# Performance work log

Measured on AMD Instinct MI355X. Metric: run time of the kernel, lower is better.

The kernel has to match this reference:

```python
import jax, jax.numpy as jnp
import numpy as np

E = 8      # num_experts
K = 2      # top-k
HID = 2048 # per-expert hidden dim


def setup_inputs() -> dict:
    key = jax.random.key(0)
    ks = jax.random.split(key, 7)
    D = 1024
    x = jax.random.normal(ks[0], (4, 2048, D), dtype=jnp.float32)
    Wr = jax.random.normal(ks[1], (D, E), dtype=jnp.float32) * 0.02
    br = jnp.zeros((E,), jnp.float32)
    W1 = jax.random.normal(ks[2], (E, D, 2 * HID), dtype=jnp.float32) * 0.02
    b1 = jnp.zeros((E, 2 * HID), jnp.float32)
    W2 = jax.random.normal(ks[3], (E, HID, D), dtype=jnp.float32) * 0.02
    b2 = jnp.zeros((E, D), jnp.float32)
    return {"x": x, "Wr": Wr, "br": br, "W1": W1, "b1": b1, "W2": W2, "b2": b2}


def reference(x, Wr, br, W1, b1, W2, b2):
    B, T, D = x.shape
    xf = x.reshape(-1, D)                               # [N, D]

    # --- router ---
    logits = xf @ Wr + br                               # [N, E]
    probs = jax.nn.softmax(logits, axis=-1)
    topk_val, topk_idx = jax.lax.top_k(logits, K)       # [N, K]
    scores = jax.nn.softmax(topk_val, axis=-1)          # [N, K]

    # --- load-balancing aux loss ---
    one_hot = jax.nn.one_hot(topk_idx, E, dtype=jnp.float32)   # [N, K, E]
    f = one_hot.sum(axis=1).mean(axis=0)                # [E] fraction routed
    p = probs.mean(axis=0)                              # [E] mean prob
    aux_loss = E * jnp.sum(jax.lax.stop_gradient(f) * p)

    # --- every expert over all tokens (faithful to naive module) ---
    h = jnp.einsum('nd,edh->enh', xf, W1) + b1[:, None, :]     # [E, N, 2H]
    a, b = h[..., :HID], h[..., HID:]
    g = jax.nn.silu(a) * b                              # swiglu, [E, N, H]
    oe = jnp.einsum('enh,ehd->end', g, W2) + b2[:, None, :]    # [E, N, D]

    # --- combine: gather each token's top-k expert outputs, weight, sum ---
    oe = oe.transpose(1, 0, 2)                          # [N, E, D]
    sel = jnp.take_along_axis(oe, topk_idx[:, :, None], axis=1)  # [N, K, D]
    out = (sel * scores[:, :, None]).sum(axis=1)        # [N, D]

    return out.reshape(B, T, D), aux_loss
```

## Files before the change

### kernel.cpp

```cpp
#include <hip/hip_runtime.h>
#include <hip/hip_bf16.h>
#include <math.h>

typedef __attribute__((ext_vector_type(8))) __bf16 bh8;
typedef __attribute__((ext_vector_type(4))) float  f4;

#define NTOK   8192
#define DIM    1024
#define HIDK   2048

#define OFF_CNT    0
#define OFF_PSUM   64
#define OFF_OFFS   128
#define OFF_ROWS   512
#define OFF_GATES  (512+262144)
#define OFF_XBF    524800
#define OFF_G      (524800+16777216)
#define OFF_W1S    (OFF_G + 68157440)
#define OFF_W2S    (OFF_W1S + 67108864)

__device__ __forceinline__ unsigned short f2bf(float x){
    union { float f; unsigned u; } v; v.f = x;
    unsigned r = v.u + 0x7FFFu + ((v.u >> 16) & 1u);
    return (unsigned short)(r >> 16);
}
__device__ __forceinline__ unsigned pk2(float a, float b){
    return (unsigned)f2bf(a) | ((unsigned)f2bf(b) << 16);
}
__device__ __forceinline__ void gload_lds16(const void* g, void* l){
    __builtin_amdgcn_global_load_lds((const __attribute__((address_space(1))) void*)g,
                                     (__attribute__((address_space(3))) void*)l, 16, 0, 0);
}

__global__ void convert_x(const float* __restrict__ x, short* __restrict__ xbf){
    size_t i = ((size_t)blockIdx.x * 256 + threadIdx.x) * 8;
    const float4* s = (const float4*)(x + i);
    float4 a = s[0], b = s[1];
    uint4 u;
    u.x = pk2(a.x, a.y); u.y = pk2(a.z, a.w);
    u.z = pk2(b.x, b.y); u.w = pk2(b.z, b.w);
    *(uint4*)(xbf + i) = u;
}

__global__ void prep_w(const float* __restrict__ W, short* __restrict__ Ws,
                       int Kdim, int Ndim){
    int kb = blockIdx.x, nb = blockIdx.y, e = blockIdx.z;
    int KB = Kdim >> 5, NB = Ndim >> 7;
    __shared__ float tile[32 * 132];
    int t = threadIdx.x;
    const float* src = W + ((size_t)(e * Kdim + kb * 32)) * Ndim + (size_t)nb * 128;
    #pragma unroll
    for (int l = 0; l < 4; l++){
        int flat = (l * 256 + t) * 4;
        int k = flat >> 7, n = flat & 127;
        float4 v = *(const float4*)(src + (size_t)k * Ndim + n);
        float* d = &tile[k * 132 + n];
        d[0] = v.x; d[1] = v.y; d[2] = v.z; d[3] = v.w;
    }
    __syncthreads();
    short* dst = Ws + (((size_t)(e * NB + nb)) * KB + kb) * 4096;
    uint out[8];
    #pragma unroll
    for (int sl = 0; sl < 2; sl++){
        int s = t * 2 + sl;
        int nl = s >> 2, pos = s & 3;
        int c = pos ^ (nl & 3) ^ ((nl >> 2) & 3);
        #pragma unroll
        for (int jj = 0; jj < 4; jj++){
            float a = tile[(c * 8 + jj * 2) * 132 + nl];
            float b = tile[(c * 8 + jj * 2 + 1) * 132 + nl];
            out[sl * 4 + jj] = pk2(a, b);
        }
    }
    *(uint4*)(dst + t * 16)     = *(uint4*)&out[0];
    *(uint4*)(dst + t * 16 + 8) = *(uint4*)&out[4];
}

__global__ void router(const float* __restrict__ x, const float* __restrict__ Wr,
                       const float* __restrict__ br,
                       int* cnt, float* psum, int* rows, float* gates){
    __shared__ float pP[8];
    __shared__ int   tE[32][2];
    __shared__ float tS[32][2];
    __shared__ int   lcnt[8], lpos[64], lexp[64], gbase[8];
    int t = threadIdx.x, lane = t & 63, w = t >> 6;
    if (t < 8){ pP[t] = 0.f; lcnt[t] = 0; }
    __syncthreads();
    int n0 = blockIdx.x * 32 + w * 8;
    for (int tk = 0; tk < 8; tk++){
        int n = n0 + tk;
        float acc[8] = {0,0,0,0,0,0,0,0};
        const float* xr = x + (size_t)n * DIM;
        for (int d = lane; d < DIM; d += 64){
            float xv = xr[d];
            const float* wrow = Wr + d * 8;
            #pragma unroll
            for (int e = 0; e < 8; e++) acc[e] += xv * wrow[e];
        }
        #pragma unroll
        for (int e = 0; e < 8; e++){
            float v = acc[e];
            v += __shfl_xor(v, 32); v += __shfl_xor(v, 16); v += __shfl_xor(v, 8);
            v += __shfl_xor(v, 4);  v += __shfl_xor(v, 2);  v += __shfl_xor(v, 1);
            acc[e] = v;
        }
        if (lane == 0){
            float l[8], ex[8], m = -1e30f;
            #pragma unroll
            for (int e = 0; e < 8; e++){ l[e] = acc[e] + br[e]; m = fmaxf(m, l[e]); }
            float s = 0.f;
            #pragma unroll
            for (int e = 0; e < 8; e++){ ex[e] = expf(l[e] - m); s += ex[e]; }
            float inv = 1.f / s;
            #pragma unroll
            for (int e = 0; e < 8; e++) atomicAdd(&pP[e], ex[e] * inv);
            int i0 = 0; float v0 = l[0];
            #pragma unroll
            for (int e = 1; e < 8; e++) if (l[e] > v0){ v0 = l[e]; i0 = e; }
            int i1 = -1; float v1 = -1e30f;
            #pragma unroll
            for (int e = 0; e < 8; e++) if (e != i0 && l[e] > v1){ v1 = l[e]; i1 = e; }
            float s0 = 1.f / (1.f + expf(v1 - v0));
            int ti = w * 8 + tk;
            tE[ti][0] = i0; tE[ti][1] = i1;
            tS[ti][0] = s0; tS[ti][1] = 1.f - s0;
        }
    }
    __syncthreads();
    if (t < 64){
        int e = tE[t >> 1][t & 1];
        lexp[t] = e;
        lpos[t] = atomicAdd(&lcnt[e], 1);
    }
    __syncthreads();
    if (t < 8){
        gbase[t] = atomicAdd(&cnt[t], lcnt[t]);
        atomicAdd(&psum[t], pP[t]);
    }
    __syncthreads();
    if (t < 64){
        int e = lexp[t];
        int p = gbase[e] + lpos[t];
        int n = blockIdx.x * 32 + (t >> 1);
        rows[e * NTOK + p]  = n;
        gates[e * NTOK + p] = tS[t >> 1][t & 1];
    }
}

__global__ void finalize_aux(const int* cnt, const float* psum, int* offs, float* out_aux){
    if (threadIdx.x == 0){
        int off = 0; float aux = 0.f;
        for (int e = 0; e < 8; e++){
            offs[e] = off; off += cnt[e];
            aux += ((float)cnt[e] * (1.f/8192.f)) * (psum[e] * (1.f/8192.f));
        }
        out_aux[0] = 8.f * aux;
    }
}

__global__ __launch_bounds__(256, 4) void gemm1(
    const short* __restrict__ xbf, const short* __restrict__ W1s,
    const float* __restrict__ b1, const int* __restrict__ cnt,
    const int* __restrict__ offs, const int* __restrict__ rows,
    short* __restrict__ g)
{
    int e = blockIdx.z;
    int Me = cnt[e];
    int mbase = blockIdx.y << 7;
    if (mbase >= Me) return;
    int xB = blockIdx.x;
    __shared__ short As[128 * 32];
    __shared__ short Bsa[64 * 32];
    __shared__ short Bsb[64 * 32];

    int t = threadIdx.x, lane = t & 63, w = t >> 6;
    int wr = w & 1, wc = w >> 1;
    int m = lane & 15, q = lane >> 4;
    int sw8 = (q ^ (m & 3) ^ ((m >> 2) & 3)) << 3;

    const int* rowsE = rows + (e << 13) + mbase;
    int r = t >> 2, pos = t & 3;
    int ca = pos ^ (r & 3) ^ ((r >> 2) & 3);
    int tok0 = (mbase + r      < Me) ? rowsE[r]      : 0;
    int tok1 = (mbase + r + 64 < Me) ? rowsE[r + 64] : 0;
    const short* ga0 = xbf + ((size_t)tok0 << 10) + (ca << 3);
    const short* ga1 = xbf + ((size_t)tok1 << 10) + (ca << 3);
    int ha = xB & 1, nb128 = xB >> 1;
    const short* gb0 = W1s + ((size_t)((e * 32 + nb128)      * 32)) * 4096 + (ha * 256 + t) * 8;
    const short* gb1 = W1s + ((size_t)((e * 32 + 16 + nb128) * 32)) * 4096 + (ha * 256 + t) * 8;
    short* ldsA0 = As  + w * 512;
    short* ldsA1 = As  + 2048 + w * 512;
    short* ldsBa = Bsa + w * 512;
    short* ldsBb = Bsb + w * 512;

    f4 acc_a[4][2], acc_b[4][2];
    f4 zz = {0.f,0.f,0.f,0.f};
    #pragma unroll
    for (int i = 0; i < 4; i++)
        #pragma unroll
        for (int j = 0; j < 2; j++){ acc_a[i][j] = zz; acc_b[i][j] = zz; }

    for (int k0 = 0; k0 < DIM; k0 += 32){
        __syncthreads();
        gload_lds16(ga0, ldsA0);
        gload_lds16(ga1, ldsA1);
        gload_lds16(gb0, ldsBa);
        gload_lds16(gb1, ldsBb);
        ga0 += 32; ga1 += 32; gb0 += 4096; gb1 += 4096;
        __syncthreads();
        bh8 av[4], ba[2], bb[2];
        #pragma unroll
        for (int i = 0; i < 4; i++)
            av[i] = *(const bh8*)&As[(wr*64 + i*16 + m) * 32 + sw8];
        #pragma unroll
        for (int j = 0; j < 2; j++){
            int nn = ((wc << 5) + j*16 + m) * 32 + sw8;
            ba[j] = *(const bh8*)&Bsa[nn];
            bb[j] = *(const bh8*)&Bsb[nn];
        }
        #pragma unroll
        for (int i = 0; i < 4; i++)
            #pragma unroll
            for (int j = 0; j < 2; j++){
                acc_a[i][j] = __builtin_amdgcn_mfma_f32_16x16x32_bf16(av[i], ba[j], acc_a[i][j], 0, 0, 0);
                acc_b[i][j] = __builtin_amdgcn_mfma_f32_16x16x32_bf16(av[i], bb[j], acc_b[i][j], 0, 0, 0);
            }
    }
    int c0 = xB << 6;
    const float* b1e = b1 + (e << 12);
    int colb = (wc << 5) + m;
    float vba[2], vbb[2];
    #pragma unroll
    for (int j = 0; j < 2; j++){
        vba[j] = b1e[c0 + colb + j*16];
        vbb[j] = b1e[HIDK + c0 + colb + j*16];
    }
    int rb = wr * 64 + (q << 2);
    short* gE = g + ((size_t)(offs[e] + mbase)) * HIDK;
    #pragma unroll
    for (int i = 0; i < 4; i++)
        #pragma unroll
        for (int reg = 0; reg < 4; reg++){
            int mr = rb + i*16 + reg;
            if (mbase + mr < Me){
                short* grow = gE + (size_t)mr * HIDK + c0 + colb;
                #pragma unroll
                for (int j = 0; j < 2; j++){
                    float va = acc_a[i][j][reg] + vba[j];
                    float vb = acc_b[i][j][reg] + vbb[j];
                    grow[j*16] = (short)f2bf(va / (1.f + __expf(-va)) * vb);
                }
            }
        }
}

__global__ __launch_bounds__(256, 4) void gemm2(
    const short* __restrict__ g, const short* __restrict__ W2s,
    const float* __restrict__ b2, const int* __restrict__ cnt,
    const int* __restrict__ offs, const int* __restrict__ rows,
    const float* __restrict__ gates, float* __restrict__ out)
{
    int e = blockIdx.z;
    int Me = cnt[e];
    int mbase = blockIdx.y << 7;
    if (mbase >= Me) return;
    int db = blockIdx.x;
    __shared__ short As[128 * 32];
    __shared__ short Bs[128 * 32];

    int t = threadIdx.x, lane = t & 63, w = t >> 6;
    int wr = w & 1, wc = w >> 1;
    int m = lane & 15, q = lane >> 4;
    int sw8 = (q ^ (m & 3) ^ ((m >> 2) & 3)) << 3;

    int gbaseR = offs[e] + mbase;
    int r = t >> 2;
    int ca = (t & 3) ^ (r & 3) ^ ((r >> 2) & 3);
    const short* ga0 = g + ((size_t)(gbaseR + r))      * HIDK + (ca << 3);
    const short* ga1 = g + ((size_t)(gbaseR + r + 64)) * HIDK + (ca << 3);
    const short* gb0 = W2s + ((size_t)((e * 8 + db) * 64)) * 4096 + t * 8;
    const short* gb1 = gb0 + 2048;
    short* ldsA0 = As + w * 512;
    short* ldsA1 = As + 2048 + w * 512;
    short* ldsB0 = Bs + w * 512;
    short* ldsB1 = Bs + 2048 + w * 512;

    f4 acc[4][4];
    f4 zz = {0.f,0.f,0.f,0.f};
    #pragma unroll
    for (int i = 0; i < 4; i++)
        #pragma unroll
        for (int j = 0; j < 4; j++) acc[i][j] = zz;

    for (int k0 = 0; k0 < HIDK; k0 += 32){
        __syncthreads();
        gload_lds16(ga0, ldsA0);
        gload_lds16(ga1, ldsA1);
        gload_lds16(gb0, ldsB0);
        gload_lds16(gb1, ldsB1);
        ga0 += 32; ga1 += 32; gb0 += 4096; gb1 += 4096;
        __syncthreads();
        bh8 av[4], bv[4];
        #pragma unroll
        for (int i = 0; i < 4; i++)
            av[i] = *(const bh8*)&As[(wr*64 + i*16 + m) * 32 + sw8];
        #pragma unroll
        for (int j = 0; j < 4; j++)
            bv[j] = *(const bh8*)&Bs[(wc*64 + j*16 + m) * 32 + sw8];
        #pragma unroll
        for (int i = 0; i < 4; i++)
            #pragma unroll
            for (int j = 0; j < 4; j++)
                acc[i][j] = __builtin_amdgcn_mfma_f32_16x16x32_bf16(av[i], bv[j], acc[i][j], 0, 0, 0);
    }
    int d0 = db << 7;
    const float* b2e = b2 + (e << 10);
    int colb = wc * 64 + m;
    float vb2[4];
    #pragma unroll
    for (int j = 0; j < 4; j++) vb2[j] = b2e[d0 + colb + j*16];
    const int* rowsE = rows + (e << 13) + mbase;
    const float* gatesE = gates + (e << 13) + mbase;
    int rb = wr * 64 + (q << 2);
    #pragma unroll
    for (int i = 0; i < 4; i++)
        #pragma unroll
        for (int reg = 0; reg < 4; reg++){
            int mr = rb + i*16 + reg;
            if (mbase + mr < Me){
                int token = rowsE[mr];
                float gate = gatesE[mr];
                float* orow = out + ((size_t)token << 10) + d0 + colb;
                #pragma unroll
                for (int j = 0; j < 4; j++)
                    unsafeAtomicAdd(&orow[j*16], gate * (acc[i][j][reg] + vb2[j]));
            }
        }
}

extern "C" void kernel_launch(void* const* d_in, const int* in_sizes, int n_in,
                              void* d_out, int out_size, void* d_ws, size_t ws_size,
                              hipStream_t stream) {
    const float* x  = (const float*)d_in[0];
    const float* Wr = (const float*)d_in[1];
    const float* br = (const float*)d_in[2];
    const float* W1 = (const float*)d_in[3];
    const float* b1 = (const float*)d_in[4];
    const float* W2 = (const float*)d_in[5];
    const float* b2 = (const float*)d_in[6];
    float* out = (float*)d_out;

    char* ws = (char*)d_ws;
    int*   cnt   = (int*)(ws + OFF_CNT);
    float* psum  = (float*)(ws + OFF_PSUM);
    int*   offs  = (int*)(ws + OFF_OFFS);
    int*   rows  = (int*)(ws + OFF_ROWS);
    float* gates = (float*)(ws + OFF_GATES);
    short* xbf   = (short*)(ws + OFF_XBF);
    short* g     = (short*)(ws + OFF_G);
    short* W1s   = (short*)(ws + OFF_W1S);
    short* W2s   = (short*)(ws + OFF_W2S);

    hipMemsetAsync(ws, 0, 192, stream);
    hipMemsetAsync(d_out, 0, (size_t)NTOK * DIM * 4, stream);

    prep_w<<<dim3(32, 32, 8), 256, 0, stream>>>(W1, W1s, 1024, 4096);
    prep_w<<<dim3(64, 8, 8),  256, 0, stream>>>(W2, W2s, 2048, 1024);
    convert_x<<<4096, 256, 0, stream>>>(x, xbf);
    router<<<256, 256, 0, stream>>>(x, Wr, br, cnt, psum, rows, gates);
    finalize_aux<<<1, 64, 0, stream>>>(cnt, psum, offs, out + (size_t)NTOK * DIM);
    gemm1<<<dim3(32, 64, 8), 256, 0, stream>>>(xbf, W1s, b1, cnt, offs, rows, g);
    gemm2<<<dim3(8, 64, 8),  256, 0, stream>>>(g, W2s, b2, cnt, offs, rows, gates, out);
}
```

Measured before the change: 673.9 us.

## Double-buffer LDS tiles in both expert GEMMs to overlap loads with MFMA

Both grouped GEMM kernels now keep two LDS buffers per operand and prefetch the next K-slice with global_load_lds while the MFMAs run on the current slice. The two __syncthreads per iteration become an inline-asm s_waitcnt vmcnt(4) plus s_barrier, and a bare barrier after compute. This is meant to hide global-memory latency behind compute. It doubles LDS use, which can lower occupancy under launch_bounds(256,4), and it depends on the hand-written vmcnt count matching the four outstanding loads per thread.

```diff
diff --git a/kernel.cpp b/kernel.cpp
--- a/kernel.cpp
+++ b/kernel.cpp
@@ -31,6 +31,9 @@
     __builtin_amdgcn_global_load_lds((const __attribute__((address_space(1))) void*)g,
                                      (__attribute__((address_space(3))) void*)l, 16, 0, 0);
 }
+#define WAITBAR_PREV() asm volatile("s_waitcnt vmcnt(4)\n\ts_barrier" ::: "memory")
+#define WAITBAR_ALL()  asm volatile("s_waitcnt vmcnt(0)\n\ts_barrier" ::: "memory")
+#define BAR_ONLY()     asm volatile("s_barrier" ::: "memory")
 
 __global__ void convert_x(const float* __restrict__ x, short* __restrict__ xbf){
     size_t i = ((size_t)blockIdx.x * 256 + threadIdx.x) * 8;
@@ -169,9 +172,9 @@
     int mbase = blockIdx.y << 7;
     if (mbase >= Me) return;
     int xB = blockIdx.x;
-    __shared__ short As[128 * 32];
-    __shared__ short Bsa[64 * 32];
-    __shared__ short Bsb[64 * 32];
+    __shared__ short As [2][4096];
+    __shared__ short Bsa[2][2048];
+    __shared__ short Bsb[2][2048];
 
     int t = threadIdx.x, lane = t & 63, w = t >> 6;
     int wr = w & 1, wc = w >> 1;
@@ -188,10 +191,10 @@
     int ha = xB & 1, nb128 = xB >> 1;
     const short* gb0 = W1s + ((size_t)((e * 32 + nb128)      * 32)) * 4096 + (ha * 256 + t) * 8;
     const short* gb1 = W1s + ((size_t)((e * 32 + 16 + nb128) * 32)) * 4096 + (ha * 256 + t) * 8;
-    short* ldsA0 = As  + w * 512;
-    short* ldsA1 = As  + 2048 + w * 512;
-    short* ldsBa = Bsa + w * 512;
-    short* ldsBb = Bsb + w * 512;
+    short* ldsA0 = &As [0][w * 512];
+    short* ldsA1 = &As [0][2048 + w * 512];
+    short* ldsBa = &Bsa[0][w * 512];
+    short* ldsBb = &Bsb[0][w * 512];
 
     f4 acc_a[4][2], acc_b[4][2];
     f4 zz = {0.f,0.f,0.f,0.f};
@@ -200,23 +203,53 @@
         #pragma unroll
         for (int j = 0; j < 2; j++){ acc_a[i][j] = zz; acc_b[i][j] = zz; }
 
-    for (int k0 = 0; k0 < DIM; k0 += 32){
-        __syncthreads();
-        gload_lds16(ga0, ldsA0);
-        gload_lds16(ga1, ldsA1);
-        gload_lds16(gb0, ldsBa);
-        gload_lds16(gb1, ldsBb);
+    gload_lds16(ga0, ldsA0);
+    gload_lds16(ga1, ldsA1);
+    gload_lds16(gb0, ldsBa);
+    gload_lds16(gb1, ldsBb);
+    ga0 += 32; ga1 += 32; gb0 += 4096; gb1 += 4096;
+
+    int cur = 0;
+    #pragma unroll 2
+    for (int k0 = 0; k0 < DIM - 32; k0 += 32){
+        int nxt = cur ^ 1;
+        gload_lds16(ga0, ldsA0 + nxt * 4096);
+        gload_lds16(ga1, ldsA1 + nxt * 4096);
+        gload_lds16(gb0, ldsBa + nxt * 2048);
+        gload_lds16(gb1, ldsBb + nxt * 2048);
         ga0 += 32; ga1 += 32; gb0 += 4096; gb1 += 4096;
-        __syncthreads();
+        WAITBAR_PREV();
         bh8 av[4], ba[2], bb[2];
         #pragma unroll
         for (int i = 0; i < 4; i++)
-            av[i] = *(const bh8*)&As[(wr*64 + i*16 + m) * 32 + sw8];
+            av[i] = *(const bh8*)&As[cur][(wr*64 + i*16 + m) * 32 + sw8];
         #pragma unroll
         for (int j = 0; j < 2; j++){
             int nn = ((wc << 5) + j*16 + m) * 32 + sw8;
-            ba[j] = *(const bh8*)&Bsa[nn];
-            bb[j] = *(const bh8*)&Bsb[nn];
+            ba[j] = *(const bh8*)&Bsa[cur][nn];
+            bb[j] = *(const bh8*)&Bsb[cur][nn];
+        }
+        #pragma unroll
+        for (int i = 0; i < 4; i++)
+            #pragma unroll
+            for (int j = 0; j < 2; j++){
+                acc_a[i][j] = __builtin_amdgcn_mfma_f32_16x16x32_bf16(av[i], ba[j], acc_a[i][j], 0, 0, 0);
+                acc_b[i][j] = __builtin_amdgcn_mfma_f32_16x16x32_bf16(av[i], bb[j], acc_b[i][j], 0, 0, 0);
+            }
+        BAR_ONLY();
+        cur = nxt;
+    }
+    WAITBAR_ALL();
+    {
+        bh8 av[4], ba[2], bb[2];
+        #pragma unroll
+        for (int i = 0; i < 4; i++)
+            av[i] = *(const bh8*)&As[cur][(wr*64 + i*16 + m) * 32 + sw8];
+        #pragma unroll
+        for (int j = 0; j < 2; j++){
+            int nn = ((wc << 5) + j*16 + m) * 32 + sw8;
+            ba[j] = *(const bh8*)&Bsa[cur][nn];
+            bb[j] = *(const bh8*)&Bsb[cur][nn];
         }
         #pragma unroll
         for (int i = 0; i < 4; i++)
@@ -265,8 +298,8 @@
     int mbase = blockIdx.y << 7;
     if (mbase >= Me) return;
     int db = blockIdx.x;
-    __shared__ short As[128 * 32];
-    __shared__ short Bs[128 * 32];
+    __shared__ short As[2][4096];
+    __shared__ short Bs[2][4096];
 
     int t = threadIdx.x, lane = t & 63, w = t >> 6;
     int wr = w & 1, wc = w >> 1;
@@ -280,10 +313,10 @@
     const short* ga1 = g + ((size_t)(gbaseR + r + 64)) * HIDK + (ca << 3);
     const short* gb0 = W2s + ((size_t)((e * 8 + db) * 64)) * 4096 + t * 8;
     const short* gb1 = gb0 + 2048;
-    short* ldsA0 = As + w * 512;
-    short* ldsA1 = As + 2048 + w * 512;
-    short* ldsB0 = Bs + w * 512;
-    short* ldsB1 = Bs + 2048 + w * 512;
+    short* ldsA0 = &As[0][w * 512];
+    short* ldsA1 = &As[0][2048 + w * 512];
+    short* ldsB0 = &Bs[0][w * 512];
+    short* ldsB1 = &Bs[0][2048 + w * 512];
 
     f4 acc[4][4];
     f4 zz = {0.f,0.f,0.f,0.f};
@@ -292,21 +325,46 @@
         #pragma unroll
         for (int j = 0; j < 4; j++) acc[i][j] = zz;
 
-    for (int k0 = 0; k0 < HIDK; k0 += 32){
-        __syncthreads();
-        gload_lds16(ga0, ldsA0);
-        gload_lds16(ga1, ldsA1);
-        gload_lds16(gb0, ldsB0);
-        gload_lds16(gb1, ldsB1);
+    gload_lds16(ga0, ldsA0);
+    gload_lds16(ga1, ldsA1);
+    gload_lds16(gb0, ldsB0);
+    gload_lds16(gb1, ldsB1);
+    ga0 += 32; ga1 += 32; gb0 += 4096; gb1 += 4096;
+
+    int cur = 0;
+    #pragma unroll 2
+    for (int k0 = 0; k0 < HIDK - 32; k0 += 32){
+        int nxt = cur ^ 1;
+        gload_lds16(ga0, ldsA0 + nxt * 4096);
+        gload_lds16(ga1, ldsA1 + nxt * 4096);
+        gload_lds16(gb0, ldsB0 + nxt * 4096);
+        gload_lds16(gb1, ldsB1 + nxt * 4096);
         ga0 += 32; ga1 += 32; gb0 += 4096; gb1 += 4096;
-        __syncthreads();
+        WAITBAR_PREV();
         bh8 av[4], bv[4];
         #pragma unroll
         for (int i = 0; i < 4; i++)
-            av[i] = *(const bh8*)&As[(wr*64 + i*16 + m) * 32 + sw8];
+            av[i] = *(const bh8*)&As[cur][(wr*64 + i*16 + m) * 32 + sw8];
         #pragma unroll
         for (int j = 0; j < 4; j++)
-            bv[j] = *(const bh8*)&Bs[(wc*64 + j*16 + m) * 32 + sw8];
+            bv[j] = *(const bh8*)&Bs[cur][(wc*64 + j*16 + m) * 32 + sw8];
+        #pragma unroll
+        for (int i = 0; i < 4; i++)
+            #pragma unroll
+            for (int j = 0; j < 4; j++)
+                acc[i][j] = __builtin_amdgcn_mfma_f32_16x16x32_bf16(av[i], bv[j], acc[i][j], 0, 0, 0);
+        BAR_ONLY();
+        cur = nxt;
+    }
+    WAITBAR_ALL();
+    {
+        bh8 av[4], bv[4];
+        #pragma unroll
+        for (int i = 0; i < 4; i++)
+            av[i] = *(const bh8*)&As[cur][(wr*64 + i*16 + m) * 32 + sw8];
+        #pragma unroll
+        for (int j = 0; j < 4; j++)
+            bv[j] = *(const bh8*)&Bs[cur][(wc*64 + j*16 + m) * 32 + sw8];
         #pragma unroll
         for (int i = 0; i < 4; i++)
             #pragma unroll
```

Result: faster. 656.1 us (-2.6%).
